# Kernel tuning notes

Measured on AMD Instinct MI355X. Metric: run time of the kernel, lower is better.

Reference implementation:

```python
import jax, jax.numpy as jnp
import numpy as np

B, D, T = 16384, 1024, 128  # batch, embed_dim, num_degradation_types
V, L = 4, 3                 # variants per sample, degradations per variant


def setup_inputs() -> dict:
    key = jax.random.key(0)
    k1, k2, k3, k4 = jax.random.split(key, 4)
    clean_embeddings = jax.random.normal(k1, (B, D), dtype=jnp.float32)
    W = jax.random.normal(k2, (T, D), dtype=jnp.float32) * (1.0 / np.sqrt(D))
    b = jnp.zeros((T,), dtype=jnp.float32)
    deg_indices = jax.random.randint(k3, (B, V, L), 0, T, dtype=jnp.int32)
    deg_mask = jax.random.randint(k4, (B, V, L), 0, 2, dtype=jnp.int32)
    return {"clean_embeddings": clean_embeddings, "W": W, "b": b,
            "deg_indices": deg_indices, "deg_mask": deg_mask}


def reference(clean_embeddings, W, b, deg_indices, deg_mask):
    # Linear + softmax: [B, T]
    logits = jnp.einsum("bd,td->bt", clean_embeddings, W) + b
    probs = jax.nn.softmax(logits, axis=-1)
    # Gather probs at each (batch, label) pair: [B, V*L] -> [B, V, L]
    flat_idx = deg_indices.reshape(B, V * L)
    gathered = jnp.take_along_axis(probs, flat_idx, axis=1).reshape(B, V, L)
    # Masked sum over all labels of a sample, divided by max(num_variants, 1)=V
    per_sample = (gathered * deg_mask.astype(probs.dtype)).sum(axis=(1, 2)) / V
    return per_sample.sum() / B
```

## Files before the change

### kernel.cpp

```cpp
#include <hip/hip_runtime.h>

#define B_SIZE 16384
#define D_DIM  1024
#define T_DIM  128
#define VLn    12
#define BM     16
#define BK     256
#define NCHUNK 4
#define GRID   (B_SIZE / BM)
#define AROWF  258
#define AROWB  1032
#define ABUFB  (BM * AROWB)
#define SLSTR  132

typedef _Float16 half8  __attribute__((ext_vector_type(8)));
typedef __fp16   fp16x2 __attribute__((ext_vector_type(2)));
typedef float    f32x4  __attribute__((ext_vector_type(4)));

union Pack16 { fp16x2 h[4]; uint4 u; half8 v; };
union Frag   { uint4 u; half8 h; };

__device__ __forceinline__ uint4 pack8u(float4 v0, float4 v1) {
    Pack16 un;
    un.h[0] = __builtin_amdgcn_cvt_pkrtz(v0.x, v0.y);
    un.h[1] = __builtin_amdgcn_cvt_pkrtz(v0.z, v0.w);
    un.h[2] = __builtin_amdgcn_cvt_pkrtz(v1.x, v1.y);
    un.h[3] = __builtin_amdgcn_cvt_pkrtz(v1.z, v1.w);
    return un.u;
}
__device__ __forceinline__ half8 pack8f(const float* fp) {
    const float2 a = ((const float2*)fp)[0];
    const float2 b = ((const float2*)fp)[1];
    const float2 c = ((const float2*)fp)[2];
    const float2 d = ((const float2*)fp)[3];
    Pack16 un;
    un.h[0] = __builtin_amdgcn_cvt_pkrtz(a.x, a.y);
    un.h[1] = __builtin_amdgcn_cvt_pkrtz(b.x, b.y);
    un.h[2] = __builtin_amdgcn_cvt_pkrtz(c.x, c.y);
    un.h[3] = __builtin_amdgcn_cvt_pkrtz(d.x, d.y);
    return un.v;
}

__device__ __forceinline__ void dma16(const float* g, void* l) {
    __builtin_amdgcn_global_load_lds(
        (__attribute__((address_space(1))) void*)g,
        (__attribute__((address_space(3))) void*)l, 16, 0, 0);
}

__global__ __launch_bounds__(256)
void conv_w(const float* __restrict__ W, uint4* __restrict__ Wf,
            float* __restrict__ out) {
    if (blockIdx.x == 0 && threadIdx.x == 0) out[0] = 0.0f;
    const int j    = blockIdx.x * 256 + threadIdx.x;
    const int kc   = j >> 10;
    const int r    = j & 1023;
    const int g    = r >> 6;
    const int lane = r & 63;
    const int n = (g & 7) * 16 + (lane & 15);
    const int k = kc * 64 + (g >> 3) * 32 + ((lane >> 4) << 3);
    const float* src = W + (size_t)n * D_DIM + k;
    Wf[j] = pack8u(*(const float4*)src, *(const float4*)(src + 4));
}

__global__ __launch_bounds__(256, 2)
void qloss_kernel(const float* __restrict__ emb,
                  const uint4* __restrict__ Wf,
                  const float* __restrict__ bias,
                  const int*   __restrict__ didx,
                  const int*   __restrict__ dmsk,
                  float*       __restrict__ out)
{
    __shared__ __align__(16) unsigned char smem[2 * ABUFB + 16];
    float* sL   = (float*)smem;
    float* sRed = (float*)(smem + 2 * ABUFB);

    const int t    = threadIdx.x;
    const int w    = t >> 6;
    const int lane = t & 63;
    const int m15  = lane & 15;
    const int quad = lane >> 4;
    const int r0   = blockIdx.x * BM;

    const float* aG0 = emb + (size_t)(r0 + 4 * w) * D_DIM + lane * 4;

    const uint4* bP = Wf + lane;
    const int CT0 = 2 * w;

    f32x4 acc[2];
    acc[0] = (f32x4){0.f, 0.f, 0.f, 0.f};
    acc[1] = (f32x4){0.f, 0.f, 0.f, 0.f};

    Frag bc[16], bn[16];

#pragma unroll
    for (int r = 0; r < 4; ++r)
        dma16(aG0 + (size_t)r * D_DIM, smem + (4 * w + r) * AROWB);
#pragma unroll
    for (int ks = 0; ks < 8; ++ks) {
        const int s = ks;
#pragma unroll
        for (int j = 0; j < 2; ++j)
            bc[ks * 2 + j].u = bP[(size_t)(s >> 1) * 1024 + ((s & 1) * 8 + CT0 + j) * 64];
    }
    asm volatile("s_waitcnt vmcnt(16)" ::: "memory");
    __builtin_amdgcn_sched_barrier(0);
    __builtin_amdgcn_s_barrier();
    __builtin_amdgcn_sched_barrier(0);

#pragma unroll
    for (int kc = 0; kc < NCHUNK; ++kc) {
        const unsigned char* bufC = smem + (kc & 1) * ABUFB;
        unsigned char*       bufN = (unsigned char*)smem + ((kc & 1) ^ 1) * ABUFB;

        if (kc + 1 < NCHUNK) {
#pragma unroll
            for (int r = 0; r < 4; ++r)
                dma16(aG0 + (size_t)r * D_DIM + (kc + 1) * BK,
                      bufN + (4 * w + r) * AROWB);
#pragma unroll
            for (int ks = 0; ks < 8; ++ks) {
                const int s = (kc + 1) * 8 + ks;
#pragma unroll
                for (int j = 0; j < 2; ++j)
                    bn[ks * 2 + j].u =
                        bP[(size_t)(s >> 1) * 1024 + ((s & 1) * 8 + CT0 + j) * 64];
            }
        }

#pragma unroll
        for (int ks = 0; ks < 8; ++ks) {
            const float* fp = (const float*)bufC + m15 * AROWF + ks * 32 + quad * 8;
            const half8 a = pack8f(fp);
            acc[0] = __builtin_amdgcn_mfma_f32_16x16x32_f16(a, bc[ks * 2 + 0].h, acc[0], 0, 0, 0);
            acc[1] = __builtin_amdgcn_mfma_f32_16x16x32_f16(a, bc[ks * 2 + 1].h, acc[1], 0, 0, 0);
        }

        if (kc + 1 < NCHUNK) {
            asm volatile("s_waitcnt vmcnt(16)" ::: "memory");
            __builtin_amdgcn_sched_barrier(0);
            __builtin_amdgcn_s_barrier();
            __builtin_amdgcn_sched_barrier(0);
#pragma unroll
            for (int q = 0; q < 16; ++q) bc[q] = bn[q];
        }
    }

    __syncthreads();
    const float b0v = bias[CT0 * 16 + m15];
    const float b1v = bias[(CT0 + 1) * 16 + m15];
#pragma unroll
    for (int i = 0; i < 4; ++i) {
        const int row = quad * 4 + i;
        sL[row * SLSTR + CT0 * 16 + m15]       = acc[0][i] + b0v;
        sL[row * SLSTR + (CT0 + 1) * 16 + m15] = acc[1][i] + b1v;
    }
    __syncthreads();

    {
        const int row = t >> 4, s = t & 15;
        float* base = &sL[row * SLSTR + s * 8];
        float v[8];
        *(float4*)&v[0] = *(const float4*)(base);
        *(float4*)&v[4] = *(const float4*)(base + 4);
        float m = -1e30f;
#pragma unroll
        for (int j = 0; j < 8; ++j) m = fmaxf(m, v[j]);
#pragma unroll
        for (int off = 1; off < 16; off <<= 1) m = fmaxf(m, __shfl_xor(m, off));
        float ssum = 0.f;
#pragma unroll
        for (int j = 0; j < 8; ++j) { v[j] = __expf(v[j] - m); ssum += v[j]; }
#pragma unroll
        for (int off = 1; off < 16; off <<= 1) ssum += __shfl_xor(ssum, off);
        const float inv = 1.0f / ssum;
#pragma unroll
        for (int j = 0; j < 8; ++j) v[j] *= inv;
        *(float4*)(base)     = *(const float4*)&v[0];
        *(float4*)(base + 4) = *(const float4*)&v[4];
    }
    __syncthreads();

    float p = 0.f;
    if (t < BM * VLn) {
        const int gi  = r0 * VLn + t;
        const int row = t / VLn;
        const int idx = didx[gi];
        const int mk  = dmsk[gi];
        p = mk ? sL[row * SLSTR + idx] : 0.f;
    }
#pragma unroll
    for (int off = 1; off < 64; off <<= 1) p += __shfl_xor(p, off);
    if (lane == 0) sRed[w] = p;
    __syncthreads();
    if (t == 0)
        atomicAdd(out, (sRed[0] + sRed[1] + sRed[2] + sRed[3]) * (1.0f / 65536.0f));
}

extern "C" void kernel_launch(void* const* d_in, const int* in_sizes, int n_in,
                              void* d_out, int out_size, void* d_ws, size_t ws_size,
                              hipStream_t stream) {
    const float* emb  = (const float*)d_in[0];
    const float* W    = (const float*)d_in[1];
    const float* bias = (const float*)d_in[2];
    const int*   didx = (const int*)d_in[3];
    const int*   dmsk = (const int*)d_in[4];
    float* out = (float*)d_out;

    uint4* Wf = (uint4*)d_ws;

    conv_w<<<64, 256, 0, stream>>>(W, Wf, out);
    qloss_kernel<<<GRID, 256, 0, stream>>>(emb, Wf, bias, didx, dmsk, out);
}
```

Measured before the change: 113.0 us.

## Double row tile to 32 with 512 threads and ring-buffer W fragment prefetch

Each block now processes 32 batch rows with 8 waves. Pairs of waves share the same W column tiles, so each W fragment loaded from global memory feeds twice as many rows. The 32-register double buffer of W fragments is replaced by a 3-slot ring that prefetches two k-steps ahead. This frees registers for higher occupancy, at the cost of more exposed per-step global load latency. LDS per block doubles, which may cap the number of resident blocks below the requested launch bound.

Measured after the change: 112.0 us. No clear change (-0.8%).

```diff
diff --git a/kernel.cpp b/kernel.cpp
--- a/kernel.cpp
+++ b/kernel.cpp
@@ -4,9 +4,10 @@
 #define D_DIM  1024
 #define T_DIM  128
 #define VLn    12
-#define BM     16
+#define BM     32
 #define BK     256
 #define NCHUNK 4
+#define NTHR   512
 #define GRID   (B_SIZE / BM)
 #define AROWF  258
 #define AROWB  1032
@@ -62,7 +63,7 @@
     Wf[j] = pack8u(*(const float4*)src, *(const float4*)(src + 4));
 }
 
-__global__ __launch_bounds__(256, 2)
+__global__ __launch_bounds__(NTHR, 4)
 void qloss_kernel(const float* __restrict__ emb,
                   const uint4* __restrict__ Wf,
                   const float* __restrict__ bias,
@@ -70,7 +71,7 @@
                   const int*   __restrict__ dmsk,
                   float*       __restrict__ out)
 {
-    __shared__ __align__(16) unsigned char smem[2 * ABUFB + 16];
+    __shared__ __align__(16) unsigned char smem[2 * ABUFB + 64];
     float* sL   = (float*)smem;
     float* sRed = (float*)(smem + 2 * ABUFB);
 
@@ -83,74 +84,72 @@
 
     const float* aG0 = emb + (size_t)(r0 + 4 * w) * D_DIM + lane * 4;
 
+    const int rg  = w >> 2;
+    const int CT0 = 2 * (w & 3);
+
     const uint4* bP = Wf + lane;
-    const int CT0 = 2 * w;
 
     f32x4 acc[2];
     acc[0] = (f32x4){0.f, 0.f, 0.f, 0.f};
     acc[1] = (f32x4){0.f, 0.f, 0.f, 0.f};
 
-    Frag bc[16], bn[16];
+    Frag bp[3][2];
+
+#define LOADB(s, slot)                                                        \
+    do {                                                                      \
+        bp[slot][0].u = bP[(size_t)((s) >> 1) * 1024 +                        \
+                           (((s) & 1) * 8 + CT0 + 0) * 64];                   \
+        bp[slot][1].u = bP[(size_t)((s) >> 1) * 1024 +                        \
+                           (((s) & 1) * 8 + CT0 + 1) * 64];                   \
+    } while (0)
 
 #pragma unroll
     for (int r = 0; r < 4; ++r)
         dma16(aG0 + (size_t)r * D_DIM, smem + (4 * w + r) * AROWB);
-#pragma unroll
-    for (int ks = 0; ks < 8; ++ks) {
-        const int s = ks;
-#pragma unroll
-        for (int j = 0; j < 2; ++j)
-            bc[ks * 2 + j].u = bP[(size_t)(s >> 1) * 1024 + ((s & 1) * 8 + CT0 + j) * 64];
-    }
-    asm volatile("s_waitcnt vmcnt(16)" ::: "memory");
+    LOADB(0, 0);
+    LOADB(1, 1);
+    asm volatile("s_waitcnt vmcnt(4)" ::: "memory");
     __builtin_amdgcn_sched_barrier(0);
     __builtin_amdgcn_s_barrier();
     __builtin_amdgcn_sched_barrier(0);
 
 #pragma unroll
     for (int kc = 0; kc < NCHUNK; ++kc) {
-        const unsigned char* bufC = smem + (kc & 1) * ABUFB;
-        unsigned char*       bufN = (unsigned char*)smem + ((kc & 1) ^ 1) * ABUFB;
+        const float* bufC = (const float*)(smem + (kc & 1) * ABUFB);
+        unsigned char* bufN = (unsigned char*)smem + ((kc & 1) ^ 1) * ABUFB;
 
         if (kc + 1 < NCHUNK) {
 #pragma unroll
             for (int r = 0; r < 4; ++r)
                 dma16(aG0 + (size_t)r * D_DIM + (kc + 1) * BK,
                       bufN + (4 * w + r) * AROWB);
-#pragma unroll
-            for (int ks = 0; ks < 8; ++ks) {
-                const int s = (kc + 1) * 8 + ks;
-#pragma unroll
-                for (int j = 0; j < 2; ++j)
-                    bn[ks * 2 + j].u =
-                        bP[(size_t)(s >> 1) * 1024 + ((s & 1) * 8 + CT0 + j) * 64];
-            }
         }
 
 #pragma unroll
         for (int ks = 0; ks < 8; ++ks) {
-            const float* fp = (const float*)bufC + m15 * AROWF + ks * 32 + quad * 8;
+            const int s = kc * 8 + ks;
+            if (s + 2 < 32) LOADB(s + 2, (s + 2) % 3);
+            const float* fp = bufC + (16 * rg + m15) * AROWF + ks * 32 + quad * 8;
             const half8 a = pack8f(fp);
-            acc[0] = __builtin_amdgcn_mfma_f32_16x16x32_f16(a, bc[ks * 2 + 0].h, acc[0], 0, 0, 0);
-            acc[1] = __builtin_amdgcn_mfma_f32_16x16x32_f16(a, bc[ks * 2 + 1].h, acc[1], 0, 0, 0);
+            acc[0] = __builtin_amdgcn_mfma_f32_16x16x32_f16(a, bp[s % 3][0].h, acc[0], 0, 0, 0);
+            acc[1] = __builtin_amdgcn_mfma_f32_16x16x32_f16(a, bp[s % 3][1].h, acc[1], 0, 0, 0);
         }
 
         if (kc + 1 < NCHUNK) {
-            asm volatile("s_waitcnt vmcnt(16)" ::: "memory");
+            asm volatile("s_waitcnt vmcnt(4)" ::: "memory");
             __builtin_amdgcn_sched_barrier(0);
             __builtin_amdgcn_s_barrier();
             __builtin_amdgcn_sched_barrier(0);
-#pragma unroll
-            for (int q = 0; q < 16; ++q) bc[q] = bn[q];
         }
     }
+#undef LOADB
 
     __syncthreads();
     const float b0v = bias[CT0 * 16 + m15];
     const float b1v = bias[(CT0 + 1) * 16 + m15];
 #pragma unroll
     for (int i = 0; i < 4; ++i) {
-        const int row = quad * 4 + i;
+        const int row = 16 * rg + quad * 4 + i;
         sL[row * SLSTR + CT0 * 16 + m15]       = acc[0][i] + b0v;
         sL[row * SLSTR + (CT0 + 1) * 16 + m15] = acc[1][i] + b1v;
     }
@@ -192,8 +191,12 @@
     for (int off = 1; off < 64; off <<= 1) p += __shfl_xor(p, off);
     if (lane == 0) sRed[w] = p;
     __syncthreads();
-    if (t == 0)
-        atomicAdd(out, (sRed[0] + sRed[1] + sRed[2] + sRed[3]) * (1.0f / 65536.0f));
+    if (t == 0) {
+        float s = 0.f;
+#pragma unroll
+        for (int i = 0; i < 8; ++i) s += sRed[i];
+        atomicAdd(out, s * (1.0f / 65536.0f));
+    }
 }
 
 extern "C" void kernel_launch(void* const* d_in, const int* in_sizes, int n_in,
@@ -209,5 +212,5 @@
     uint4* Wf = (uint4*)d_ws;
 
     conv_w<<<64, 256, 0, stream>>>(W, Wf, out);
-    qloss_kernel<<<GRID, 256, 0, stream>>>(emb, Wf, bias, didx, dmsk, out);
-}
+    qloss_kernel<<<GRID, NTHR, 0, stream>>>(emb, Wf, bias, didx, dmsk, out);
+}
```
